# Optimization experiments

Measured on AMD Instinct MI355X. Metric: run time of the kernel, lower is better.

Reference implementation:

```python
import jax, jax.numpy as jnp
import numpy as np

B, D_MODEL, H = 2048, 1024, 16
D_K = D_MODEL // H


def setup_inputs() -> dict:
    root = jax.random.key(0)
    ks = jax.random.split(root, 11)
    w_scale = 1.0 / np.sqrt(D_MODEL).astype(np.float32)
    inp = {
        "query": jax.random.normal(ks[0], (B, D_MODEL), jnp.float32),
        "key": jax.random.normal(ks[1], (B, D_MODEL), jnp.float32),
        "value": jax.random.normal(ks[2], (B, D_MODEL), jnp.float32),
        # Linear weights (used as x @ W + b)
        "Wq": jax.random.normal(ks[3], (D_MODEL, D_MODEL), jnp.float32) * w_scale,
        "bq": jnp.zeros((D_MODEL,), jnp.float32),
        "Wk": jax.random.normal(ks[4], (D_MODEL, D_MODEL), jnp.float32) * w_scale,
        "bk": jnp.zeros((D_MODEL,), jnp.float32),
        "Wv": jax.random.normal(ks[5], (D_MODEL, D_MODEL), jnp.float32) * w_scale,
        "bv": jnp.zeros((D_MODEL,), jnp.float32),
        # Random U drawn fresh each forward in torch; materialized here for determinism.
        # torch shape: randn(d_model, nbatches*d_k).view(nbatches, h, d_k, d_k)
        "U": jax.random.normal(ks[6], (B, H, D_K, D_K), jnp.float32),
    }
    return inp


def reference(query, key, value, Wq, bq, Wk, bk, Wv, bv, U):
    b, dm = query.shape
    h = U.shape[1]
    dk = dm // h
    residual = key
    # QKV projections, then view(b, -1, h, dk).transpose(1, 2) -> [b, h, 1, dk]
    q = (query @ Wq + bq).reshape(b, 1, h, dk).transpose(0, 2, 1, 3)
    k = (key @ Wk + bk).reshape(b, 1, h, dk).transpose(0, 2, 1, 3)
    v = (value @ Wv + bv).reshape(b, 1, h, dk).transpose(0, 2, 1, 3)
    # attn_weight = (q @ U) @ k^T : [b,h,1,dk] @ [b,h,dk,dk] @ [b,h,dk,1] -> [b,h,1,1]
    aw = jnp.matmul(q, U)
    scores = jnp.matmul(aw, jnp.swapaxes(k, -1, -2))
    p = jax.nn.softmax(scores, axis=-1)  # dropout is identity at inference
    # context = p^T @ v : [b,h,1,1] @ [b,h,1,dk] -> [b,h,1,dk]
    ctx = jnp.matmul(jnp.swapaxes(p, -1, -2), v)
    ctx = jnp.swapaxes(ctx, 1, 2).reshape(b, dm)
    return ctx + residual
```

## Files before the change

### kernel.cpp

```cpp
#include <hip/hip_runtime.h>
#include <hip/hip_bf16.h>


#define M_DIM 2048
#define N_DIM 1024
#define K_DIM 1024

typedef __attribute__((ext_vector_type(8))) short short8;
typedef __attribute__((ext_vector_type(4))) float f32x4;

constexpr int BM = 64, BN = 64, BK = 64;
constexpr int THREADS = 256;

__device__ inline unsigned int rne_bf16(float f) {
    unsigned u = __builtin_bit_cast(unsigned, f);
    return (u + 0x7FFFu + ((u >> 16) & 1u)) >> 16;
}
__device__ inline unsigned int pack2(float lo, float hi) {
    return rne_bf16(lo) | (rne_bf16(hi) << 16);
}

__global__ __launch_bounds__(THREADS)
void vproj_residual_kernel(const float* __restrict__ key,
                           const float* __restrict__ value,
                           const float* __restrict__ Wv,
                           const float* __restrict__ bv,
                           float* __restrict__ out) {
    __shared__ __align__(16) short As[BM * BK];
    __shared__ __align__(16) short Bs[BN * BK];

    const int tid = threadIdx.x;
    const int bn = blockIdx.x;
    const int bm = blockIdx.y;
    const int row0 = bm * BM;
    const int col0 = bn * BN;

    const int wid = tid >> 6;
    const int lane = tid & 63;
    const int wr = wid >> 1;
    const int wc = wid & 1;

    f32x4 acc[2][2] = {};

    const int arow = tid >> 2;
    const int ak0 = (tid & 3) * 16;
    const int achunk0 = (tid & 3) * 2;
    const int asw = arow & 7;

    const int bj = (tid & 15) * 4;
    const int bkp = tid >> 4;

    for (int kt = 0; kt < K_DIM / BK; ++kt) {
        {
            const float* ap = value + (size_t)(row0 + arow) * K_DIM + kt * BK + ak0;
            f32x4 a0 = *(const f32x4*)(ap + 0);
            f32x4 a1 = *(const f32x4*)(ap + 4);
            f32x4 a2 = *(const f32x4*)(ap + 8);
            f32x4 a3 = *(const f32x4*)(ap + 12);
            union { short8 s; unsigned u[4]; } c0, c1;
            c0.u[0] = pack2(a0[0], a0[1]);
            c0.u[1] = pack2(a0[2], a0[3]);
            c0.u[2] = pack2(a1[0], a1[1]);
            c0.u[3] = pack2(a1[2], a1[3]);
            c1.u[0] = pack2(a2[0], a2[1]);
            c1.u[1] = pack2(a2[2], a2[3]);
            c1.u[2] = pack2(a3[0], a3[1]);
            c1.u[3] = pack2(a3[2], a3[3]);
            *(short8*)(&As[arow * 64 + (((achunk0 + 0) ^ asw) << 3)]) = c0.s;
            *(short8*)(&As[arow * 64 + (((achunk0 + 1) ^ asw) << 3)]) = c1.s;
        }
        #pragma unroll
        for (int s = 0; s < 2; ++s) {
            int kp = bkp + s * 16;
            int krow = kt * BK + 2 * kp;
            const float* bp = Wv + (size_t)krow * N_DIM + col0 + bj;
            f32x4 b0 = *(const f32x4*)(bp);
            f32x4 b1 = *(const f32x4*)(bp + N_DIM);
            unsigned* bsu = (unsigned*)Bs;
            #pragma unroll
            for (int m = 0; m < 4; ++m) {
                unsigned u = pack2(b0[m], b1[m]);
                int n = bj + m;
                int chunk = (kp >> 2) ^ ((n >> 1) & 7);
                bsu[n * 32 + (chunk << 2) + (kp & 3)] = u;
            }
        }
        __syncthreads();

        #pragma unroll
        for (int ks = 0; ks < 2; ++ks) {
            short8 afr[2], bfr[2];
            #pragma unroll
            for (int fm = 0; fm < 2; ++fm) {
                int r = wr * 32 + fm * 16 + (lane & 15);
                int chunk = (ks * 4 + (lane >> 4)) ^ (r & 7);
                afr[fm] = *(const short8*)(&As[r * 64 + (chunk << 3)]);
            }
            #pragma unroll
            for (int fn = 0; fn < 2; ++fn) {
                int n = wc * 32 + fn * 16 + (lane & 15);
                int chunk = (ks * 4 + (lane >> 4)) ^ ((n >> 1) & 7);
                bfr[fn] = *(const short8*)(&Bs[n * 64 + (chunk << 3)]);
            }
            #pragma unroll
            for (int fm = 0; fm < 2; ++fm)
                #pragma unroll
                for (int fn = 0; fn < 2; ++fn)
                    acc[fm][fn] = __builtin_amdgcn_mfma_f32_16x16x32_bf16(
                        afr[fm], bfr[fn], acc[fm][fn], 0, 0, 0);
        }
        __syncthreads();
    }

    #pragma unroll
    for (int fm = 0; fm < 2; ++fm) {
        #pragma unroll
        for (int fn = 0; fn < 2; ++fn) {
            int col = col0 + wc * 32 + fn * 16 + (lane & 15);
            int rbase = row0 + wr * 32 + fm * 16 + ((lane >> 4) * 4);
            float b = bv[col];
            #pragma unroll
            for (int i = 0; i < 4; ++i) {
                int r = rbase + i;
                out[(size_t)r * N_DIM + col] = acc[fm][fn][i] + b + key[(size_t)r * N_DIM + col];
            }
        }
    }
}

extern "C" void kernel_launch(void* const* d_in, const int* in_sizes, int n_in,
                              void* d_out, int out_size, void* d_ws, size_t ws_size,
                              hipStream_t stream) {
    const float* key   = (const float*)d_in[1];
    const float* value = (const float*)d_in[2];
    const float* Wv    = (const float*)d_in[7];
    const float* bv    = (const float*)d_in[8];
    float* out = (float*)d_out;

    dim3 grid(N_DIM / BN, M_DIM / BM);
    dim3 block(THREADS);
    vproj_residual_kernel<<<grid, block, 0, stream>>>(key, value, Wv, bv, out);
}
```

Before: 25.51 us.

## Pre-convert operands to swizzled bf16 tiles and stream GEMM via direct LDS loads

A separate conversion kernel now turns value and Wv into bf16 once. It writes them to workspace in a pre-tiled, XOR-swizzled layout, with Wv transposed. The GEMM kernel then copies whole tiles straight into LDS with global_load_lds, double-buffered so the next k-tile loads while MFMAs run on the current one. This removes the repeated fp32 loads and per-tile conversion inside the GEMM inner loop. The cost is a second kernel launch and an extra round trip of the bf16 data through workspace memory.

```diff
diff --git a/kernel.cpp b/kernel.cpp
--- a/kernel.cpp
+++ b/kernel.cpp
@@ -9,98 +9,110 @@
 typedef __attribute__((ext_vector_type(8))) short short8;
 typedef __attribute__((ext_vector_type(4))) float f32x4;
 
-constexpr int BM = 64, BN = 64, BK = 64;
-constexpr int THREADS = 256;
-
-__device__ inline unsigned int rne_bf16(float f) {
+__device__ inline unsigned rne_bf16(float f) {
     unsigned u = __builtin_bit_cast(unsigned, f);
     return (u + 0x7FFFu + ((u >> 16) & 1u)) >> 16;
 }
-__device__ inline unsigned int pack2(float lo, float hi) {
+__device__ inline unsigned pack2(float lo, float hi) {
     return rne_bf16(lo) | (rne_bf16(hi) << 16);
 }
 
-__global__ __launch_bounds__(THREADS)
-void vproj_residual_kernel(const float* __restrict__ key,
-                           const float* __restrict__ value,
-                           const float* __restrict__ Wv,
-                           const float* __restrict__ bv,
-                           float* __restrict__ out) {
-    __shared__ __align__(16) short As[BM * BK];
-    __shared__ __align__(16) short Bs[BN * BK];
+__global__ __launch_bounds__(256)
+void convert_kernel(const float* __restrict__ value, const float* __restrict__ Wv,
+                    short* __restrict__ Vb, short* __restrict__ WvTb) {
+    __shared__ unsigned tr[64 * 33];
+    const int b = blockIdx.x, tid = threadIdx.x;
+    if (b < 1024) {
+        int g = b * 256 + tid;
+        int row = g >> 7, ch = g & 127;
+        int kt = ch >> 3, c = ch & 7;
+        int tm = row >> 6, r = row & 63;
+        const float* p = value + (size_t)row * K_DIM + ch * 8;
+        f32x4 a0 = *(const f32x4*)p;
+        f32x4 a1 = *(const f32x4*)(p + 4);
+        union { short8 s; unsigned u[4]; } o;
+        o.u[0] = pack2(a0[0], a0[1]);
+        o.u[1] = pack2(a0[2], a0[3]);
+        o.u[2] = pack2(a1[0], a1[1]);
+        o.u[3] = pack2(a1[2], a1[3]);
+        *(short8*)&Vb[(size_t)(tm * 16 + kt) * 4096 + r * 64 + ((c ^ (r & 7)) << 3)] = o.s;
+    } else {
+        int b2 = b - 1024;
+        int tn = b2 & 15, kt = b2 >> 4;
+        #pragma unroll
+        for (int s = 0; s < 2; ++s) {
+            int kp = (tid >> 4) + s * 16;
+            int n4 = (tid & 15) * 4;
+            const float* bp = Wv + (size_t)(kt * 64 + 2 * kp) * N_DIM + tn * 64 + n4;
+            f32x4 b0 = *(const f32x4*)bp;
+            f32x4 b1 = *(const f32x4*)(bp + N_DIM);
+            #pragma unroll
+            for (int m = 0; m < 4; ++m)
+                tr[(n4 + m) * 33 + kp] = pack2(b0[m], b1[m]);
+        }
+        __syncthreads();
+        int n = tid >> 2;
+        #pragma unroll
+        for (int h = 0; h < 2; ++h) {
+            int c = (tid & 3) + 4 * h;
+            union { short8 s; unsigned u[4]; } o;
+            #pragma unroll
+            for (int p = 0; p < 4; ++p)
+                o.u[p] = tr[n * 33 + c * 4 + p];
+            *(short8*)&WvTb[(size_t)(tn * 16 + kt) * 4096 + n * 64 + ((c ^ (n & 7)) << 3)] = o.s;
+        }
+    }
+}
+
+__device__ inline void gl_lds16(const short* g, short* l) {
+    __builtin_amdgcn_global_load_lds((const __attribute__((address_space(1))) void*)g,
+                                     (__attribute__((address_space(3))) void*)l,
+                                     16, 0, 0);
+}
+
+__global__ __launch_bounds__(256)
+void gemm_kernel(const short* __restrict__ Vb, const short* __restrict__ WvTb,
+                 const float* __restrict__ key, const float* __restrict__ bv,
+                 float* __restrict__ out) {
+    __shared__ __align__(16) short As[2][4096];
+    __shared__ __align__(16) short Bs[2][4096];
 
     const int tid = threadIdx.x;
     const int bn = blockIdx.x;
     const int bm = blockIdx.y;
-    const int row0 = bm * BM;
-    const int col0 = bn * BN;
-
+    const int lane = tid & 63;
     const int wid = tid >> 6;
-    const int lane = tid & 63;
     const int wr = wid >> 1;
     const int wc = wid & 1;
 
+    const short* Abase = Vb + (size_t)bm * 16 * 4096;
+    const short* Bbase = WvTb + (size_t)bn * 16 * 4096;
+
     f32x4 acc[2][2] = {};
 
-    const int arow = tid >> 2;
-    const int ak0 = (tid & 3) * 16;
-    const int achunk0 = (tid & 3) * 2;
-    const int asw = arow & 7;
+    auto stage = [&](int buf, int kt) {
+        const short* ga = Abase + (size_t)kt * 4096 + tid * 8;
+        const short* gb = Bbase + (size_t)kt * 4096 + tid * 8;
+        gl_lds16(ga,        &As[buf][tid * 8]);
+        gl_lds16(ga + 2048, &As[buf][2048 + tid * 8]);
+        gl_lds16(gb,        &Bs[buf][tid * 8]);
+        gl_lds16(gb + 2048, &Bs[buf][2048 + tid * 8]);
+    };
 
-    const int bj = (tid & 15) * 4;
-    const int bkp = tid >> 4;
-
-    for (int kt = 0; kt < K_DIM / BK; ++kt) {
-        {
-            const float* ap = value + (size_t)(row0 + arow) * K_DIM + kt * BK + ak0;
-            f32x4 a0 = *(const f32x4*)(ap + 0);
-            f32x4 a1 = *(const f32x4*)(ap + 4);
-            f32x4 a2 = *(const f32x4*)(ap + 8);
-            f32x4 a3 = *(const f32x4*)(ap + 12);
-            union { short8 s; unsigned u[4]; } c0, c1;
-            c0.u[0] = pack2(a0[0], a0[1]);
-            c0.u[1] = pack2(a0[2], a0[3]);
-            c0.u[2] = pack2(a1[0], a1[1]);
-            c0.u[3] = pack2(a1[2], a1[3]);
-            c1.u[0] = pack2(a2[0], a2[1]);
-            c1.u[1] = pack2(a2[2], a2[3]);
-            c1.u[2] = pack2(a3[0], a3[1]);
-            c1.u[3] = pack2(a3[2], a3[3]);
-            *(short8*)(&As[arow * 64 + (((achunk0 + 0) ^ asw) << 3)]) = c0.s;
-            *(short8*)(&As[arow * 64 + (((achunk0 + 1) ^ asw) << 3)]) = c1.s;
-        }
-        #pragma unroll
-        for (int s = 0; s < 2; ++s) {
-            int kp = bkp + s * 16;
-            int krow = kt * BK + 2 * kp;
-            const float* bp = Wv + (size_t)krow * N_DIM + col0 + bj;
-            f32x4 b0 = *(const f32x4*)(bp);
-            f32x4 b1 = *(const f32x4*)(bp + N_DIM);
-            unsigned* bsu = (unsigned*)Bs;
-            #pragma unroll
-            for (int m = 0; m < 4; ++m) {
-                unsigned u = pack2(b0[m], b1[m]);
-                int n = bj + m;
-                int chunk = (kp >> 2) ^ ((n >> 1) & 7);
-                bsu[n * 32 + (chunk << 2) + (kp & 3)] = u;
-            }
-        }
-        __syncthreads();
-
+    auto compute = [&](int buf) {
         #pragma unroll
         for (int ks = 0; ks < 2; ++ks) {
             short8 afr[2], bfr[2];
+            const int g = ks * 4 + (lane >> 4);
             #pragma unroll
             for (int fm = 0; fm < 2; ++fm) {
                 int r = wr * 32 + fm * 16 + (lane & 15);
-                int chunk = (ks * 4 + (lane >> 4)) ^ (r & 7);
-                afr[fm] = *(const short8*)(&As[r * 64 + (chunk << 3)]);
+                afr[fm] = *(const short8*)&As[buf][r * 64 + ((g ^ (r & 7)) << 3)];
             }
             #pragma unroll
             for (int fn = 0; fn < 2; ++fn) {
                 int n = wc * 32 + fn * 16 + (lane & 15);
-                int chunk = (ks * 4 + (lane >> 4)) ^ ((n >> 1) & 7);
-                bfr[fn] = *(const short8*)(&Bs[n * 64 + (chunk << 3)]);
+                bfr[fn] = *(const short8*)&Bs[buf][n * 64 + ((g ^ (n & 7)) << 3)];
             }
             #pragma unroll
             for (int fm = 0; fm < 2; ++fm)
@@ -109,9 +121,18 @@
                     acc[fm][fn] = __builtin_amdgcn_mfma_f32_16x16x32_bf16(
                         afr[fm], bfr[fn], acc[fm][fn], 0, 0, 0);
         }
+    };
+
+    stage(0, 0);
+    __syncthreads();
+    #pragma unroll 1
+    for (int kt = 0; kt < 16; ++kt) {
+        if (kt < 15) stage((kt + 1) & 1, kt + 1);
+        compute(kt & 1);
         __syncthreads();
     }
 
+    const int row0 = bm * 64, col0 = bn * 64;
     #pragma unroll
     for (int fm = 0; fm < 2; ++fm) {
         #pragma unroll
@@ -137,7 +158,9 @@
     const float* bv    = (const float*)d_in[8];
     float* out = (float*)d_out;
 
-    dim3 grid(N_DIM / BN, M_DIM / BM);
-    dim3 block(THREADS);
-    vproj_residual_kernel<<<grid, block, 0, stream>>>(key, value, Wv, bv, out);
+    short* Vb   = (short*)d_ws;
+    short* WvTb = (short*)d_ws + (size_t)M_DIM * N_DIM;
+
+    convert_kernel<<<1024 + 256, 256, 0, stream>>>(value, Wv, Vb, WvTb);
+    gemm_kernel<<<dim3(N_DIM / 64, M_DIM / 64), 256, 0, stream>>>(Vb, WvTb, key, bv, out);
 }
```

Result: faster. 23.42 us (-8.2%).
